# Kernel optimization log

Hardware: AMD Instinct MI355X
Metric: run time of the kernel (lower is better)

The kernel has to match this reference:

```python
import jax, jax.numpy as jnp
from jax import lax
import numpy as np

BATCH = 131072
D_IN = 512
D_OUT = 512
ITERS = 10
THRES = 1e-6


def bjorck_orthonormalize(w, iters=ITERS, thres=THRES):
    """Order-1 Bjorck orthonormalization: W <- 1.5*W - 0.5*W (W^T W).

    Row-orthogonal if out<=in, column-orthogonal otherwise (operate on W^T).
    Early-stops when max|delta| <= thres, matching the module's tolerance.
    """
    transpose = w.shape[0] > w.shape[1]
    if transpose:
        w = w.T

    def cond(state):
        i, _, err = state
        return jnp.logical_and(i < iters, err > thres)

    def body(state):
        i, w, _ = state
        w_new = 1.5 * w - 0.5 * (w @ (w.T @ w))
        err = jnp.max(jnp.abs(w_new - w))
        return i + 1, w_new, err

    _, w, _ = lax.while_loop(
        cond, body, (jnp.array(0, jnp.int32), w, jnp.array(jnp.inf, w.dtype))
    )
    if transpose:
        w = w.T
    return w


def setup_inputs() -> dict:
    key = jax.random.key(0)
    k1, k2 = jax.random.split(key)
    inputs = jax.random.normal(k1, (BATCH, D_IN), dtype=jnp.float32)
    # scaled Gaussian so singular values lie in (0, sqrt(3)) -> Bjorck converges
    weight = jax.random.normal(k2, (D_OUT, D_IN), dtype=jnp.float32) * (0.5 / np.sqrt(D_IN))
    return {"inputs": inputs, "weight": weight}


def reference(inputs, weight):
    # training-mode forward with projection=True, inverse=False:
    # weight.data <- bjorck(weight.data); out = F.linear(inputs, weight)
    w_proj = bjorck_orthonormalize(weight)
    return inputs @ w_proj.T  # [batch, out_features]
```

## Files before the change

kernel.cpp:

```cpp
#include <hip/hip_runtime.h>


using bf16x8 = __attribute__((ext_vector_type(8))) short;
using f32x4  = __attribute__((ext_vector_type(4))) float;
using u16x8  = __attribute__((ext_vector_type(8))) unsigned short;

#define DI 512
#define MFMA16(a, b, c) __builtin_amdgcn_mfma_f32_16x16x32_bf16(a, b, c, 0, 0, 0)
#define SXS 520

__device__ __forceinline__ unsigned short f2bf(float f) {
  unsigned int u = __builtin_bit_cast(unsigned int, f);
  u += 0x7FFFu + ((u >> 16) & 1u);
  return (unsigned short)(u >> 16);
}
__device__ __forceinline__ float bf2f(unsigned short h) {
  unsigned int u = ((unsigned int)h) << 16;
  return __builtin_bit_cast(float, u);
}

__global__ void k_split(const float* __restrict__ W, float* __restrict__ Wm,
                        unsigned short* __restrict__ Wh, unsigned short* __restrict__ Wl,
                        unsigned short* __restrict__ WTh, unsigned short* __restrict__ WTl) {
  int idx = blockIdx.x * blockDim.x + threadIdx.x;
  int m = idx >> 9, i = idx & 511;
  float w = W[idx];
  Wm[idx] = w;
  unsigned short h  = f2bf(w);
  unsigned short lo = f2bf(w - bf2f(h));
  Wh[idx] = h; Wl[idx] = lo;
  WTh[i * DI + m] = h; WTl[i * DI + m] = lo;
}

__global__ __launch_bounds__(256) void k_mm2(
    const unsigned short* __restrict__ Ah, const unsigned short* __restrict__ Al,
    const unsigned short* __restrict__ Bh, const unsigned short* __restrict__ Bl,
    int mode,
    const float* __restrict__ Wm_in, float* __restrict__ Wm_out,
    unsigned short* __restrict__ Oh, unsigned short* __restrict__ Ol,
    unsigned short* __restrict__ OTh, unsigned short* __restrict__ OTl) {
  const int tid = threadIdx.x;
  const int l = tid & 63, lw = tid >> 6;
  const int wid = (blockIdx.x << 2) | lw;
  const int tile = wid >> 1, half = wid & 1;
  const int m0 = (tile >> 5) << 4, n0 = (tile & 31) << 4;
  const int kb = half << 8;
  const int lm = l & 15, lk = l >> 4;
  const int ra = (m0 + lm) * DI + kb + (lk << 3);
  const int rb = (n0 + lm) * DI + kb + (lk << 3);

  __shared__ f32x4 red[2][64];
  const int pr = lw >> 1;

  f32x4 a0{}, a1{}, a2{}, a3{}, a4{}, a5{};
#pragma unroll
  for (int k0 = 0; k0 < 256; k0 += 64) {
    bf16x8 ah0 = *(const bf16x8*)&Ah[ra + k0];
    bf16x8 al0 = *(const bf16x8*)&Al[ra + k0];
    bf16x8 bh0 = *(const bf16x8*)&Bh[rb + k0];
    bf16x8 bl0 = *(const bf16x8*)&Bl[rb + k0];
    bf16x8 ah1 = *(const bf16x8*)&Ah[ra + k0 + 32];
    bf16x8 al1 = *(const bf16x8*)&Al[ra + k0 + 32];
    bf16x8 bh1 = *(const bf16x8*)&Bh[rb + k0 + 32];
    bf16x8 bl1 = *(const bf16x8*)&Bl[rb + k0 + 32];
    a0 = MFMA16(ah0, bh0, a0);
    a1 = MFMA16(ah0, bl0, a1);
    a2 = MFMA16(al0, bh0, a2);
    a3 = MFMA16(ah1, bh1, a3);
    a4 = MFMA16(ah1, bl1, a4);
    a5 = MFMA16(al1, bh1, a5);
  }
  f32x4 acc = (a0 + a1) + (a2 + a3) + (a4 + a5);

  if (half) red[pr][l] = acc;
  __syncthreads();
  if (!half) {
    acc += red[pr][l];
    const int r0 = m0 + (lk << 2);
    const int cn = n0 + lm;
#pragma unroll
    for (int r = 0; r < 4; ++r) {
      const int gm = r0 + r, gn = cn;
      const float v = acc[r];
      if (mode == 0) {
        unsigned short h = f2bf(v);
        Oh[gm * DI + gn] = h;
        Ol[gm * DI + gn] = f2bf(v - bf2f(h));
      } else if (mode == 1) {
        const float wn = 1.5f * Wm_in[gm * DI + gn] - 0.5f * v;
        Wm_out[gm * DI + gn] = wn;
        unsigned short h = f2bf(wn), lo = f2bf(wn - bf2f(h));
        Oh[gm * DI + gn] = h;   Ol[gm * DI + gn] = lo;
        OTh[gn * DI + gm] = h;  OTl[gn * DI + gm] = lo;
      } else {
        const float wn = 1.5f * Wm_in[gm * DI + gn] - 0.5f * v;
        Oh[gm * DI + gn] = f2bf(wn);
      }
    }
  }
}

__global__ __launch_bounds__(512, 4) void k_big(
    const float* __restrict__ X, const unsigned short* __restrict__ Wp,
    float* __restrict__ out) {
  __shared__ unsigned short sX[64 * SXS];
  const int tid = threadIdx.x;
  const int wv = tid >> 6, l = tid & 63;
  const int lm = l & 15, lk = l >> 4;
  const int rowbase = blockIdx.x << 6;

  {
    const int xrow = tid >> 3;
    const int ci = tid & 7;
    const float* xp = &X[(rowbase + xrow) * DI];
#pragma unroll
    for (int i = 0; i < 8; ++i) {
      const int c = ci + (i << 3);
      f32x4 v0 = *(const f32x4*)(xp + c * 8);
      f32x4 v1 = *(const f32x4*)(xp + c * 8 + 4);
      u16x8 h;
      h[0] = f2bf(v0[0]); h[1] = f2bf(v0[1]); h[2] = f2bf(v0[2]); h[3] = f2bf(v0[3]);
      h[4] = f2bf(v1[0]); h[5] = f2bf(v1[1]); h[6] = f2bf(v1[2]); h[7] = f2bf(v1[3]);
      *(u16x8*)&sX[xrow * SXS + c * 8] = h;
    }
  }
  __syncthreads();

  f32x4 acc[4][4] = {};
  const unsigned short* wbase = &Wp[(((wv << 6) + lm) * DI) + (lk << 3)];
#pragma unroll 4
  for (int k = 0; k < 16; ++k) {
    bf16x8 b[4], a[4];
#pragma unroll
    for (int nf = 0; nf < 4; ++nf)
      b[nf] = *(const bf16x8*)&wbase[((nf << 4) * DI) + (k << 5)];
#pragma unroll
    for (int mf = 0; mf < 4; ++mf)
      a[mf] = *(const bf16x8*)&sX[((mf << 4) + lm) * SXS + (k << 5) + (lk << 3)];
#pragma unroll
    for (int mf = 0; mf < 4; ++mf)
#pragma unroll
      for (int nf = 0; nf < 4; ++nf)
        acc[mf][nf] = MFMA16(b[nf], a[mf], acc[mf][nf]);
  }

#pragma unroll
  for (int mf = 0; mf < 4; ++mf) {
    const int gm = rowbase + (mf << 4) + lm;
#pragma unroll
    for (int nf = 0; nf < 4; ++nf) {
      const int gn = (wv << 6) + (nf << 4) + (lk << 2);
      *(f32x4*)&out[gm * DI + gn] = acc[mf][nf];
    }
  }
}

extern "C" void kernel_launch(void* const* d_in, const int* in_sizes, int n_in,
                              void* d_out, int out_size, void* d_ws, size_t ws_size,
                              hipStream_t stream) {
  const float* X = (const float*)d_in[0];
  const float* W = (const float*)d_in[1];
  float* out = (float*)d_out;

  char* ws = (char*)d_ws;
  size_t off = 0;
  auto carve = [&](size_t bytes) { void* p = ws + off; off += (bytes + 255) & ~(size_t)255; return p; };

  const size_t F32 = (size_t)DI * DI * 4;
  const size_t BF  = (size_t)DI * DI * 2;

  float* Wm[2];           unsigned short *Wh[2], *Wl[2], *WTh[2], *WTl[2];
  Wm[0]  = (float*)carve(F32);          Wm[1]  = (float*)carve(F32);
  Wh[0]  = (unsigned short*)carve(BF);  Wh[1]  = (unsigned short*)carve(BF);
  Wl[0]  = (unsigned short*)carve(BF);  Wl[1]  = (unsigned short*)carve(BF);
  WTh[0] = (unsigned short*)carve(BF);  WTh[1] = (unsigned short*)carve(BF);
  WTl[0] = (unsigned short*)carve(BF);  WTl[1] = (unsigned short*)carve(BF);
  unsigned short* Gh = (unsigned short*)carve(BF);
  unsigned short* Gl = (unsigned short*)carve(BF);

  k_split<<<1024, 256, 0, stream>>>(W, Wm[0], Wh[0], Wl[0], WTh[0], WTl[0]);

  int cur = 0;
  for (int it = 0; it < 10; ++it) {
    k_mm2<<<512, 256, 0, stream>>>(WTh[cur], WTl[cur], WTh[cur], WTl[cur], 0,
                                   nullptr, nullptr, Gh, Gl, nullptr, nullptr);
    const int nxt = cur ^ 1;
    k_mm2<<<512, 256, 0, stream>>>(Wh[cur], Wl[cur], Gh, Gl, (it == 9) ? 2 : 1,
                                   Wm[cur], Wm[nxt], Wh[nxt], Wl[nxt], WTh[nxt], WTl[nxt]);
    cur = nxt;
  }

  k_big<<<2048, 512, 0, stream>>>(X, Wh[cur], out);
}
```

Measured before the change: 423.1 us.

## Pipeline big GEMM with swizzled LDS double staging and drop fp32 weight copy

Restructures the main X·Wᵀ kernel to 256-thread blocks, each wave computing a 64x128 output tile. X and W k-slices are staged through swizzled shared memory, and the next slice's global loads are prefetched during the current MFMAs. Outputs use nontemporal stores. The Bjorck iterations no longer keep an fp32 master copy and rebuild W from its bf16 hi+lo split, which removes fp32 reads and writes but slightly changes precision.

```diff
diff --git a/kernel.cpp b/kernel.cpp
--- a/kernel.cpp
+++ b/kernel.cpp
@@ -7,7 +7,6 @@
 
 #define DI 512
 #define MFMA16(a, b, c) __builtin_amdgcn_mfma_f32_16x16x32_bf16(a, b, c, 0, 0, 0)
-#define SXS 520
 
 __device__ __forceinline__ unsigned short f2bf(float f) {
   unsigned int u = __builtin_bit_cast(unsigned int, f);
@@ -19,13 +18,12 @@
   return __builtin_bit_cast(float, u);
 }
 
-__global__ void k_split(const float* __restrict__ W, float* __restrict__ Wm,
+__global__ void k_split(const float* __restrict__ W,
                         unsigned short* __restrict__ Wh, unsigned short* __restrict__ Wl,
                         unsigned short* __restrict__ WTh, unsigned short* __restrict__ WTl) {
   int idx = blockIdx.x * blockDim.x + threadIdx.x;
   int m = idx >> 9, i = idx & 511;
   float w = W[idx];
-  Wm[idx] = w;
   unsigned short h  = f2bf(w);
   unsigned short lo = f2bf(w - bf2f(h));
   Wh[idx] = h; Wl[idx] = lo;
@@ -36,7 +34,6 @@
     const unsigned short* __restrict__ Ah, const unsigned short* __restrict__ Al,
     const unsigned short* __restrict__ Bh, const unsigned short* __restrict__ Bl,
     int mode,
-    const float* __restrict__ Wm_in, float* __restrict__ Wm_out,
     unsigned short* __restrict__ Oh, unsigned short* __restrict__ Ol,
     unsigned short* __restrict__ OTh, unsigned short* __restrict__ OTl) {
   const int tid = threadIdx.x;
@@ -86,71 +83,99 @@
         unsigned short h = f2bf(v);
         Oh[gm * DI + gn] = h;
         Ol[gm * DI + gn] = f2bf(v - bf2f(h));
-      } else if (mode == 1) {
-        const float wn = 1.5f * Wm_in[gm * DI + gn] - 0.5f * v;
-        Wm_out[gm * DI + gn] = wn;
-        unsigned short h = f2bf(wn), lo = f2bf(wn - bf2f(h));
-        Oh[gm * DI + gn] = h;   Ol[gm * DI + gn] = lo;
-        OTh[gn * DI + gm] = h;  OTl[gn * DI + gm] = lo;
       } else {
-        const float wn = 1.5f * Wm_in[gm * DI + gn] - 0.5f * v;
-        Oh[gm * DI + gn] = f2bf(wn);
+        const float wcur = bf2f(Ah[gm * DI + gn]) + bf2f(Al[gm * DI + gn]);
+        const float wn = 1.5f * wcur - 0.5f * v;
+        if (mode == 1) {
+          unsigned short h = f2bf(wn), lo = f2bf(wn - bf2f(h));
+          Oh[gm * DI + gn] = h;   Ol[gm * DI + gn] = lo;
+          OTh[gn * DI + gm] = h;  OTl[gn * DI + gm] = lo;
+        } else {
+          Oh[gm * DI + gn] = f2bf(wn);
+        }
       }
     }
   }
 }
 
-__global__ __launch_bounds__(512, 4) void k_big(
+__global__ __launch_bounds__(256, 2) void k_big(
     const float* __restrict__ X, const unsigned short* __restrict__ Wp,
     float* __restrict__ out) {
-  __shared__ unsigned short sX[64 * SXS];
+  __shared__ unsigned short sX[2048];
+  __shared__ unsigned short sB[16384];
   const int tid = threadIdx.x;
-  const int wv = tid >> 6, l = tid & 63;
+  const int w = tid >> 6, l = tid & 63;
   const int lm = l & 15, lk = l >> 4;
+  const int ck = lk ^ ((lm >> 1) & 3);
   const int rowbase = blockIdx.x << 6;
 
-  {
-    const int xrow = tid >> 3;
-    const int ci = tid & 7;
-    const float* xp = &X[(rowbase + xrow) * DI];
-#pragma unroll
-    for (int i = 0; i < 8; ++i) {
-      const int c = ci + (i << 3);
-      f32x4 v0 = *(const f32x4*)(xp + c * 8);
-      f32x4 v1 = *(const f32x4*)(xp + c * 8 + 4);
-      u16x8 h;
-      h[0] = f2bf(v0[0]); h[1] = f2bf(v0[1]); h[2] = f2bf(v0[2]); h[3] = f2bf(v0[3]);
-      h[4] = f2bf(v1[0]); h[5] = f2bf(v1[1]); h[6] = f2bf(v1[2]); h[7] = f2bf(v1[3]);
-      *(u16x8*)&sX[xrow * SXS + c * 8] = h;
-    }
-  }
-  __syncthreads();
-
-  f32x4 acc[4][4] = {};
-  const unsigned short* wbase = &Wp[(((wv << 6) + lm) * DI) + (lk << 3)];
-#pragma unroll 4
+  const int arow = tid >> 2, ac = tid & 3;
+  const int alds = (arow * 4 + (ac ^ ((arow >> 1) & 3))) * 8;
+  const float* xsrc = &X[(rowbase + arow) * DI + (ac << 3)];
+
+  const int brow_l = l >> 2;
+  const int bcs = (l & 3) ^ ((brow_l >> 1) & 3);
+
+  f32x4 acc[4][8] = {};
+  f32x4 xr0, xr1;
+  u16x8 wr[8];
+
+  auto issue = [&](int kk) {
+    xr0 = *(const f32x4*)(xsrc + (kk << 5));
+    xr1 = *(const f32x4*)(xsrc + (kk << 5) + 4);
+#pragma unroll
+    for (int ph = 0; ph < 8; ++ph) {
+      const int rowblk = ph * 64 + w * 16;
+      wr[ph] = *(const u16x8*)&Wp[(rowblk + brow_l) * DI + (kk << 5) + (bcs << 3)];
+    }
+  };
+  auto publish = [&]() {
+    u16x8 h;
+    h[0] = f2bf(xr0[0]); h[1] = f2bf(xr0[1]); h[2] = f2bf(xr0[2]); h[3] = f2bf(xr0[3]);
+    h[4] = f2bf(xr1[0]); h[5] = f2bf(xr1[1]); h[6] = f2bf(xr1[2]); h[7] = f2bf(xr1[3]);
+    *(u16x8*)&sX[alds] = h;
+#pragma unroll
+    for (int ph = 0; ph < 8; ++ph)
+      *(u16x8*)&sB[(ph * 64 + w * 16) * 32 + l * 8] = wr[ph];
+  };
+
+  issue(0);
+  asm volatile("s_waitcnt vmcnt(0)" ::: "memory");
+  publish();
+  asm volatile("s_waitcnt lgkmcnt(0)" ::: "memory");
+  __builtin_amdgcn_s_barrier();
+
   for (int k = 0; k < 16; ++k) {
-    bf16x8 b[4], a[4];
-#pragma unroll
-    for (int nf = 0; nf < 4; ++nf)
-      b[nf] = *(const bf16x8*)&wbase[((nf << 4) * DI) + (k << 5)];
+    if (k < 15) issue(k + 1);
+    bf16x8 a[4], b[8];
 #pragma unroll
     for (int mf = 0; mf < 4; ++mf)
-      a[mf] = *(const bf16x8*)&sX[((mf << 4) + lm) * SXS + (k << 5) + (lk << 3)];
+      a[mf] = *(const bf16x8*)&sX[((mf * 16 + lm) * 4 + ck) * 8];
+#pragma unroll
+    for (int nf = 0; nf < 8; ++nf)
+      b[nf] = *(const bf16x8*)&sB[((w * 128 + nf * 16 + lm) * 4 + ck) * 8];
 #pragma unroll
     for (int mf = 0; mf < 4; ++mf)
 #pragma unroll
-      for (int nf = 0; nf < 4; ++nf)
+      for (int nf = 0; nf < 8; ++nf)
         acc[mf][nf] = MFMA16(b[nf], a[mf], acc[mf][nf]);
+    if (k < 15) {
+      asm volatile("s_waitcnt lgkmcnt(0)" ::: "memory");
+      __builtin_amdgcn_s_barrier();
+      asm volatile("s_waitcnt vmcnt(0)" ::: "memory");
+      publish();
+      asm volatile("s_waitcnt lgkmcnt(0)" ::: "memory");
+      __builtin_amdgcn_s_barrier();
+    }
   }
 
 #pragma unroll
   for (int mf = 0; mf < 4; ++mf) {
     const int gm = rowbase + (mf << 4) + lm;
 #pragma unroll
-    for (int nf = 0; nf < 4; ++nf) {
-      const int gn = (wv << 6) + (nf << 4) + (lk << 2);
-      *(f32x4*)&out[gm * DI + gn] = acc[mf][nf];
+    for (int nf = 0; nf < 8; ++nf) {
+      const int gn = (w << 7) + (nf << 4) + (lk << 2);
+      __builtin_nontemporal_store(acc[mf][nf], (f32x4*)&out[gm * DI + gn]);
     }
   }
 }
@@ -166,11 +191,9 @@
   size_t off = 0;
   auto carve = [&](size_t bytes) { void* p = ws + off; off += (bytes + 255) & ~(size_t)255; return p; };
 
-  const size_t F32 = (size_t)DI * DI * 4;
-  const size_t BF  = (size_t)DI * DI * 2;
-
-  float* Wm[2];           unsigned short *Wh[2], *Wl[2], *WTh[2], *WTl[2];
-  Wm[0]  = (float*)carve(F32);          Wm[1]  = (float*)carve(F32);
+  const size_t BF = (size_t)DI * DI * 2;
+
+  unsigned short *Wh[2], *Wl[2], *WTh[2], *WTl[2];
   Wh[0]  = (unsigned short*)carve(BF);  Wh[1]  = (unsigned short*)carve(BF);
   Wl[0]  = (unsigned short*)carve(BF);  Wl[1]  = (unsigned short*)carve(BF);
   WTh[0] = (unsigned short*)carve(BF);  WTh[1] = (unsigned short*)carve(BF);
@@ -178,17 +201,17 @@
   unsigned short* Gh = (unsigned short*)carve(BF);
   unsigned short* Gl = (unsigned short*)carve(BF);
 
-  k_split<<<1024, 256, 0, stream>>>(W, Wm[0], Wh[0], Wl[0], WTh[0], WTl[0]);
+  k_split<<<1024, 256, 0, stream>>>(W, Wh[0], Wl[0], WTh[0], WTl[0]);
 
   int cur = 0;
   for (int it = 0; it < 10; ++it) {
     k_mm2<<<512, 256, 0, stream>>>(WTh[cur], WTl[cur], WTh[cur], WTl[cur], 0,
-                                   nullptr, nullptr, Gh, Gl, nullptr, nullptr);
+                                   Gh, Gl, nullptr, nullptr);
     const int nxt = cur ^ 1;
     k_mm2<<<512, 256, 0, stream>>>(Wh[cur], Wl[cur], Gh, Gl, (it == 9) ? 2 : 1,
-                                   Wm[cur], Wm[nxt], Wh[nxt], Wl[nxt], WTh[nxt], WTl[nxt]);
+                                   Wh[nxt], Wl[nxt], WTh[nxt], WTl[nxt]);
     cur = nxt;
   }
 
-  k_big<<<2048, 512, 0, stream>>>(X, Wh[cur], out);
-}
+  k_big<<<2048, 256, 0, stream>>>(X, Wh[cur], out);
+}
```

Measured after the change: 402.8 us. 1.05x faster.
